# Kernel tuning notes

Measured on AMD Instinct MI355X. Metric: run time of the kernel, lower is better.

## Reference

```python
import jax, jax.numpy as jnp
import numpy as np

D_MODEL = 1024
N_HEADS = 16
HEAD_DIM = D_MODEL // N_HEADS
SEQ_LEN = 2048
D_FF = 4 * D_MODEL
LCC_SCALE = 0.1
LN_EPS = 1e-5
NORM_EPS = 1e-12  # F.normalize eps


def _layer_norm(x, g, b):
    mu = jnp.mean(x, axis=-1, keepdims=True)
    var = jnp.mean(jnp.square(x - mu), axis=-1, keepdims=True)
    return (x - mu) * jax.lax.rsqrt(var + LN_EPS) * g + b


def setup_inputs() -> dict:
    key = jax.random.key(0)
    ks = jax.random.split(key, 8)
    s = 0.02  # weight init scale
    return {
        "x": jax.random.normal(ks[0], (SEQ_LEN, D_MODEL), jnp.float32),
        "lcc_values": jax.random.uniform(ks[1], (SEQ_LEN,), jnp.float32),
        "w_qkv": jax.random.normal(ks[2], (D_MODEL, 3 * D_MODEL), jnp.float32) * s,
        "b_qkv": jnp.zeros((3 * D_MODEL,), jnp.float32),
        "w_out": jax.random.normal(ks[3], (D_MODEL, D_MODEL), jnp.float32) * s,
        "b_out": jnp.zeros((D_MODEL,), jnp.float32),
        "ln1_g": jnp.ones((D_MODEL,), jnp.float32),
        "ln1_b": jnp.zeros((D_MODEL,), jnp.float32),
        "ln2_g": jnp.ones((D_MODEL,), jnp.float32),
        "ln2_b": jnp.zeros((D_MODEL,), jnp.float32),
        "w_ff1": jax.random.normal(ks[4], (D_MODEL, D_FF), jnp.float32) * s,
        "b_ff1": jnp.zeros((D_FF,), jnp.float32),
        "w_ff2": jax.random.normal(ks[5], (D_FF, D_MODEL), jnp.float32) * s,
        "b_ff2": jnp.zeros((D_MODEL,), jnp.float32),
    }


def reference(x, lcc_values, w_qkv, b_qkv, w_out, b_out, ln1_g, ln1_b,
              ln2_g, ln2_b, w_ff1, b_ff1, w_ff2, b_ff2):
    L = x.shape[0]
    scaling = HEAD_DIM ** -0.5

    normed = _layer_norm(x, ln1_g, ln1_b)
    qkv = normed @ w_qkv + b_qkv                      # [L, 3D]
    qkv = qkv.reshape(L, 3, N_HEADS, HEAD_DIM)
    q = jnp.transpose(qkv[:, 0], (1, 0, 2))           # [H, L, d]
    k = jnp.transpose(qkv[:, 1], (1, 0, 2))
    v = jnp.transpose(qkv[:, 2], (1, 0, 2))

    # cosine attention: L2-normalize q, k
    q = q / jnp.maximum(jnp.linalg.norm(q, axis=-1, keepdims=True), NORM_EPS)
    k = k / jnp.maximum(jnp.linalg.norm(k, axis=-1, keepdims=True), NORM_EPS)
    q = q * scaling

    scores = jnp.einsum('hld,hmd->hlm', q, k)         # [H, L, L]
    bias = (lcc_values[:, None] + lcc_values[None, :]) * 0.5 * LCC_SCALE
    scores = jnp.clip(scores + bias[None], -10.0, 10.0)
    probs = jax.nn.softmax(scores, axis=-1)

    attn = jnp.einsum('hlm,hmd->hld', probs, v)       # [H, L, d]
    attn = jnp.transpose(attn, (1, 0, 2)).reshape(L, D_MODEL)
    x = x + (attn @ w_out + b_out)

    normed2 = _layer_norm(x, ln2_g, ln2_b)
    h = jax.nn.gelu(normed2 @ w_ff1 + b_ff1, approximate=False)
    x = x + (h @ w_ff2 + b_ff2)
    return x
```

## Files before the change

kernel.cpp:

```cpp
#include <hip/hip_runtime.h>
#include <hip/hip_bf16.h>

#define D_MODEL 1024
#define SEQ 2048
#define NH 16
#define HD 64
#define DFF 4096

typedef __attribute__((ext_vector_type(8))) __bf16 bf16x8;
typedef __attribute__((ext_vector_type(4))) float f32x4;

__device__ __forceinline__ unsigned short f2bf(float f) {
    union { float f; unsigned u; } v; v.f = f;
    unsigned r = v.u + 0x7fffu + ((v.u >> 16) & 1u);
    return (unsigned short)(r >> 16);
}
__device__ __forceinline__ unsigned pack2(float a, float b) {
    return (unsigned)f2bf(a) | ((unsigned)f2bf(b) << 16);
}
__device__ __forceinline__ float bf2f(unsigned short u) {
    union { unsigned u; float f; } v; v.u = ((unsigned)u) << 16;
    return v.f;
}
__device__ __forceinline__ bf16x8 ld_frag(const unsigned short* p) {
    union { uint4 u; bf16x8 b; } c;
    c.u = *(const uint4*)p;
    return c.b;
}

typedef __attribute__((address_space(3))) unsigned lds_u32;
typedef const __attribute__((address_space(1))) unsigned glob_u32;
__device__ __forceinline__ void gl_lds16(const unsigned short* g, unsigned short* l) {
    __builtin_amdgcn_global_load_lds((glob_u32*)g, (lds_u32*)l, 16, 0, 0);
}

#define MFMA16(a,b,c) __builtin_amdgcn_mfma_f32_16x16x32_bf16(a,b,c,0,0,0)

__global__ __launch_bounds__(256) void wcast_all(const float* __restrict__ wq, const float* __restrict__ wo,
                                                 const float* __restrict__ wf1, const float* __restrict__ wf2,
                                                 unsigned short* __restrict__ oq, unsigned short* __restrict__ oo,
                                                 unsigned short* __restrict__ of1, unsigned short* __restrict__ of2) {
    __shared__ unsigned short lt[64][72];
    int id = blockIdx.x;
    const float* W; unsigned short* O; int K, N, nb, kb;
    if (id < 768)       { W = wq;  O = oq;  K = 1024; N = 3072; nb = id % 48; kb = id / 48; }
    else if (id < 1024) { id -= 768;  W = wo;  O = oo;  K = 1024; N = 1024; nb = id & 15; kb = id >> 4; }
    else if (id < 2048) { id -= 1024; W = wf1; O = of1; K = 1024; N = 4096; nb = id & 63; kb = id >> 6; }
    else                { id -= 2048; W = wf2; O = of2; K = 4096; N = 1024; nb = id & 15; kb = id >> 4; }
    int t = threadIdx.x;
    int r = t >> 2, c0 = (t & 3) << 4;
    const float* src = W + (size_t)(kb*64 + r) * N + nb*64 + c0;
    float4 f0 = ((const float4*)src)[0];
    float4 f1 = ((const float4*)src)[1];
    float4 f2 = ((const float4*)src)[2];
    float4 f3 = ((const float4*)src)[3];
    unsigned* dst = (unsigned*)&lt[r][c0];
    dst[0]=pack2(f0.x,f0.y); dst[1]=pack2(f0.z,f0.w);
    dst[2]=pack2(f1.x,f1.y); dst[3]=pack2(f1.z,f1.w);
    dst[4]=pack2(f2.x,f2.y); dst[5]=pack2(f2.z,f2.w);
    dst[6]=pack2(f3.x,f3.y); dst[7]=pack2(f3.z,f3.w);
    __syncthreads();
    int n_ = t >> 2, k0 = (t & 3) << 4;
    unsigned obuf[8];
#pragma unroll
    for (int i = 0; i < 8; i++)
        obuf[i] = (unsigned)lt[k0 + 2*i][n_] | ((unsigned)lt[k0 + 2*i + 1][n_] << 16);
    unsigned short* out = O + (size_t)(nb*64 + n_) * K + kb*64 + k0;
    ((uint4*)out)[0] = *(uint4*)&obuf[0];
    ((uint4*)out)[1] = *(uint4*)&obuf[4];
}

__global__ __launch_bounds__(256) void ln_kernel(const float* __restrict__ x,
                                                 const float* __restrict__ g,
                                                 const float* __restrict__ b,
                                                 unsigned short* __restrict__ out) {
    int row = blockIdx.x, t = threadIdx.x;
    float4 v = ((const float4*)(x + (size_t)row * D_MODEL))[t];
    float s  = v.x + v.y + v.z + v.w;
    float sq = v.x*v.x + v.y*v.y + v.z*v.z + v.w*v.w;
#pragma unroll
    for (int m = 1; m < 64; m <<= 1) { s += __shfl_xor(s, m, 64); sq += __shfl_xor(sq, m, 64); }
    __shared__ float ls[4], lq[4];
    int wave = t >> 6, lane = t & 63;
    if (lane == 0) { ls[wave] = s; lq[wave] = sq; }
    __syncthreads();
    s  = ls[0]+ls[1]+ls[2]+ls[3];
    sq = lq[0]+lq[1]+lq[2]+lq[3];
    float mu  = s * (1.0f / D_MODEL);
    float var = sq * (1.0f / D_MODEL) - mu * mu;
    float rs  = rsqrtf(var + 1e-5f);
    int c = t * 4;
    float y0 = (v.x - mu) * rs * g[c+0] + b[c+0];
    float y1 = (v.y - mu) * rs * g[c+1] + b[c+1];
    float y2 = (v.z - mu) * rs * g[c+2] + b[c+2];
    float y3 = (v.w - mu) * rs * g[c+3] + b[c+3];
    unsigned* o = (unsigned*)(out + (size_t)row * D_MODEL + c);
    o[0] = pack2(y0, y1); o[1] = pack2(y2, y3);
}

__global__ __launch_bounds__(256) void reduce_ln(const float* __restrict__ x,
                                                 const float* __restrict__ bout,
                                                 const unsigned short* __restrict__ parts,
                                                 const float* __restrict__ g,
                                                 const float* __restrict__ b,
                                                 float* __restrict__ x1,
                                                 unsigned short* __restrict__ x2n) {
    int row = blockIdx.x, t = threadIdx.x;
    int i = row * 256 + t;
    float4 v = ((const float4*)x)[i];
    float4 bb = ((const float4*)bout)[t];
    v.x += bb.x; v.y += bb.y; v.z += bb.z; v.w += bb.w;
    ushort4 u0 = ((const ushort4*)parts)[i];
    ushort4 u1 = ((const ushort4*)(parts + (size_t)SEQ*D_MODEL))[i];
    v.x += bf2f(u0.x) + bf2f(u1.x);
    v.y += bf2f(u0.y) + bf2f(u1.y);
    v.z += bf2f(u0.z) + bf2f(u1.z);
    v.w += bf2f(u0.w) + bf2f(u1.w);
    ((float4*)x1)[i] = v;
    float s  = v.x + v.y + v.z + v.w;
    float sq = v.x*v.x + v.y*v.y + v.z*v.z + v.w*v.w;
#pragma unroll
    for (int m = 1; m < 64; m <<= 1) { s += __shfl_xor(s, m, 64); sq += __shfl_xor(sq, m, 64); }
    __shared__ float ls[4], lq[4];
    int wave = t >> 6, lane = t & 63;
    if (lane == 0) { ls[wave] = s; lq[wave] = sq; }
    __syncthreads();
    s  = ls[0]+ls[1]+ls[2]+ls[3];
    sq = lq[0]+lq[1]+lq[2]+lq[3];
    float mu  = s * (1.0f / D_MODEL);
    float var = sq * (1.0f / D_MODEL) - mu * mu;
    float rs  = rsqrtf(var + 1e-5f);
    int c = t * 4;
    float y0 = (v.x - mu) * rs * g[c+0] + b[c+0];
    float y1 = (v.y - mu) * rs * g[c+1] + b[c+1];
    float y2 = (v.z - mu) * rs * g[c+2] + b[c+2];
    float y3 = (v.w - mu) * rs * g[c+3] + b[c+3];
    unsigned* o = (unsigned*)(x2n + (size_t)row * D_MODEL + c);
    o[0] = pack2(y0, y1); o[1] = pack2(y2, y3);
}

__global__ __launch_bounds__(256) void reduce_ff2(const float* __restrict__ res,
                                                  const float* __restrict__ bias,
                                                  const unsigned short* __restrict__ parts,
                                                  float* __restrict__ out) {
    int i = blockIdx.x * 256 + threadIdx.x;
    float4 r = ((const float4*)res)[i];
    float4 b = ((const float4*)bias)[i & (D_MODEL/4 - 1)];
    r.x += b.x; r.y += b.y; r.z += b.z; r.w += b.w;
#pragma unroll
    for (int p = 0; p < 4; p++) {
        ushort4 u = ((const ushort4*)(parts + (size_t)p * SEQ * D_MODEL))[i];
        r.x += bf2f(u.x); r.y += bf2f(u.y); r.z += bf2f(u.z); r.w += bf2f(u.w);
    }
    ((float4*)out)[i] = r;
}

#define TMg 128
#define TNg 128
#define SMEM_U16 (2 * (TMg + TNg) * 64)
__device__ __forceinline__ void gemm_core(const unsigned short* __restrict__ A,
                                          const unsigned short* __restrict__ Bt,
                                          int K, int K0, int KS, int bm, int bn,
                                          unsigned short* smem, f32x4 acc[4][4],
                                          int wave, int lane) {
    constexpr int AI = 4, BI = 4, MI = 4, NI = 4;
    constexpr int HALF = (TMg + TNg) * 64;
    int quad = lane >> 4, lr = lane & 15;

    const unsigned short* pa[AI];
    int aoff[AI];
#pragma unroll
    for (int i = 0; i < AI; i++) {
        int rl = wave*32 + i*8 + (lane >> 3);
        int ss = (lane & 7) ^ (rl & 7);
        pa[i] = A + (size_t)(bm*TMg + rl) * K + K0 + ss*8;
        aoff[i] = (wave*32 + i*8) * 64;
    }
    const unsigned short* pb[BI];
    int boff[BI];
#pragma unroll
    for (int i = 0; i < BI; i++) {
        int rl = wave*32 + i*8 + (lane >> 3);
        int ss = (lane & 7) ^ (rl & 7);
        pb[i] = Bt + (size_t)(bn*TNg + rl) * K + K0 + ss*8;
        boff[i] = TMg*64 + (wave*32 + i*8) * 64;
    }

    int wr = (wave >> 1) * 64, wc = (wave & 1) * 64;
    int foA[2][MI], foB[2][NI];
#pragma unroll
    for (int i = 0; i < MI; i++) {
        int row = wr + i*16 + lr;
        foA[0][i] = row*64 + ((quad     ^ (row & 7)))*8;
        foA[1][i] = row*64 + (((quad+4) ^ (row & 7)))*8;
    }
#pragma unroll
    for (int j = 0; j < NI; j++) {
        int row = wc + j*16 + lr;
        foB[0][j] = TMg*64 + row*64 + ((quad     ^ (row & 7)))*8;
        foB[1][j] = TMg*64 + row*64 + (((quad+4) ^ (row & 7)))*8;
    }

#pragma unroll
    for (int i = 0; i < AI; i++) gl_lds16(pa[i], smem + aoff[i]);
#pragma unroll
    for (int i = 0; i < BI; i++) gl_lds16(pb[i], smem + boff[i]);

    int bo = 0;
    for (int kk = 0; kk < KS; kk += 64) {
        __syncthreads();
        if (kk + 64 < KS) {
            int nb = bo ^ HALF;
#pragma unroll
            for (int i = 0; i < AI; i++) gl_lds16(pa[i] + kk + 64, smem + nb + aoff[i]);
#pragma unroll
            for (int i = 0; i < BI; i++) gl_lds16(pb[i] + kk + 64, smem + nb + boff[i]);
        }
#pragma unroll
        for (int h = 0; h < 2; h++) {
            bf16x8 af[MI], bfr[NI];
#pragma unroll
            for (int i = 0; i < MI; i++) af[i]  = ld_frag(smem + bo + foA[h][i]);
#pragma unroll
            for (int j = 0; j < NI; j++) bfr[j] = ld_frag(smem + bo + foB[h][j]);
#pragma unroll
            for (int i = 0; i < MI; i++)
#pragma unroll
                for (int j = 0; j < NI; j++)
                    acc[i][j] = MFMA16(af[i], bfr[j], acc[i][j]);
        }
        bo ^= HALF;
    }
}

__device__ __forceinline__ void acc_init(f32x4 acc[4][4]) {
    f32x4 z = {0.f, 0.f, 0.f, 0.f};
#pragma unroll
    for (int i = 0; i < 4; i++)
#pragma unroll
        for (int j = 0; j < 4; j++) acc[i][j] = z;
}

__global__ __launch_bounds__(256) void k_gemm_qkv(const unsigned short* __restrict__ A,
                                                  const unsigned short* __restrict__ Bt,
                                                  const float* __restrict__ bias,
                                                  unsigned short* __restrict__ qn,
                                                  unsigned short* __restrict__ kn,
                                                  unsigned short* __restrict__ vt) {
    __shared__ unsigned short smem[SMEM_U16];
    int t = threadIdx.x;
    int bn = blockIdx.x, bm = blockIdx.y;
    int wave = t >> 6, lane = t & 63;
    int quad = lane >> 4, lr = lane & 15;
    f32x4 acc[4][4];
    acc_init(acc);
    gemm_core(A, Bt, 1024, 0, 1024, bm, bn, smem, acc, wave, lane);

    int wr = (wave >> 1) * 64, wc = (wave & 1) * 64;
    int sec = bn >> 3, hp = bn & 7;
    float bv[4];
#pragma unroll
    for (int j = 0; j < 4; j++) bv[j] = bias[bn*TNg + wc + j*16 + lr];
#pragma unroll
    for (int i = 0; i < 4; i++)
#pragma unroll
        for (int j = 0; j < 4; j++)
#pragma unroll
            for (int r = 0; r < 4; r++) acc[i][j][r] += bv[j];

    if (sec < 2) {
        int h = hp*2 + (wave & 1);
        unsigned short* dst = (sec == 0) ? qn : kn;
        float mul = (sec == 0) ? 0.125f : 1.0f;
#pragma unroll
        for (int i = 0; i < 4; i++)
#pragma unroll
            for (int r = 0; r < 4; r++) {
                float ss = 0.f;
#pragma unroll
                for (int j = 0; j < 4; j++) ss += acc[i][j][r]*acc[i][j][r];
                ss += __shfl_xor(ss, 1, 64); ss += __shfl_xor(ss, 2, 64);
                ss += __shfl_xor(ss, 4, 64); ss += __shfl_xor(ss, 8, 64);
                float scale = mul / fmaxf(sqrtf(ss), 1e-12f);
                int row = bm*TMg + wr + i*16 + quad*4 + r;
                size_t base = ((size_t)h*SEQ + row) * HD;
#pragma unroll
                for (int j = 0; j < 4; j++)
                    dst[base + j*16 + lr] = f2bf(acc[i][j][r] * scale);
            }
    } else {
        __syncthreads();
        unsigned short (*lv)[136] = (unsigned short (*)[136])smem;
#pragma unroll
        for (int i = 0; i < 4; i++)
#pragma unroll
            for (int j = 0; j < 4; j++)
#pragma unroll
                for (int r = 0; r < 4; r++)
                    lv[wc + j*16 + lr][wr + i*16 + quad*4 + r] = f2bf(acc[i][j][r]);
        __syncthreads();
        int d = t >> 1, l0 = (t & 1) * 64;
        unsigned short* ov = vt + ((size_t)(hp*128 + d)) * SEQ + bm*TMg + l0;
#pragma unroll
        for (int c = 0; c < 8; c++)
            ((uint4*)ov)[c] = *(uint4*)&lv[d][l0 + c*8];
    }
}

template<int SPLITK>
__device__ __forceinline__ void gemm_part(const unsigned short* A, const unsigned short* Bt,
                                          unsigned short* C, int M, int N, int K) {
    __shared__ unsigned short smem[SMEM_U16];
    int t = threadIdx.x;
    int bn = blockIdx.x, bm = blockIdx.y, kz = blockIdx.z;
    int wave = t >> 6, lane = t & 63;
    int quad = lane >> 4, lr = lane & 15;
    int KS = K / SPLITK;
    f32x4 acc[4][4];
    acc_init(acc);
    gemm_core(A, Bt, K, kz*KS, KS, bm, bn, smem, acc, wave, lane);
    int wr = (wave >> 1) * 64, wc = (wave & 1) * 64;
    unsigned short* P = C + (size_t)kz * M * N;
#pragma unroll
    for (int i = 0; i < 4; i++)
#pragma unroll
        for (int j = 0; j < 4; j++) {
            int row0 = bm*TMg + wr + i*16 + quad*4;
            int col  = bn*TNg + wc + j*16 + lr;
#pragma unroll
            for (int r = 0; r < 4; r++)
                P[(size_t)(row0 + r) * N + col] = f2bf(acc[i][j][r]);
        }
}
__global__ __launch_bounds__(256) void k_gemm_op(const unsigned short* A, const unsigned short* Bt,
                                                 unsigned short* C, int M, int N, int K) {
    gemm_part<2>(A, Bt, C, M, N, K);
}
__global__ __launch_bounds__(256) void k_gemm_ff2(const unsigned short* A, const unsigned short* Bt,
                                                  unsigned short* C, int M, int N, int K) {
    gemm_part<4>(A, Bt, C, M, N, K);
}

__global__ __launch_bounds__(256) void k_gemm_ff1(const unsigned short* __restrict__ A,
                                                  const unsigned short* __restrict__ Bt,
                                                  const float* __restrict__ bias,
                                                  unsigned short* __restrict__ C,
                                                  int M, int N, int K) {
    __shared__ unsigned short smem[SMEM_U16];
    int t = threadIdx.x;
    int bn = blockIdx.x, bm = blockIdx.y;
    int wave = t >> 6, lane = t & 63;
    int quad = lane >> 4, lr = lane & 15;
    f32x4 acc[4][4];
    acc_init(acc);
    gemm_core(A, Bt, K, 0, K, bm, bn, smem, acc, wave, lane);
    int wr = (wave >> 1) * 64, wc = (wave & 1) * 64;
#pragma unroll
    for (int i = 0; i < 4; i++)
#pragma unroll
        for (int j = 0; j < 4; j++) {
            int row0 = bm*TMg + wr + i*16 + quad*4;
            int col  = bn*TNg + wc + j*16 + lr;
            float bvv = bias[col];
#pragma unroll
            for (int r = 0; r < 4; r++) {
                float v = acc[i][j][r] + bvv;
                v = 0.5f * v * (1.0f + erff(v * 0.70710678118654752f));
                C[(size_t)(row0 + r) * N + col] = f2bf(v);
            }
        }
}

#define KSPLIT 2
#define KTILES (SEQ / 64 / KSPLIT)
__global__ __launch_bounds__(256) void attn_kernel(const unsigned short* __restrict__ qn,
                                                   const unsigned short* __restrict__ kn,
                                                   const unsigned short* __restrict__ vt,
                                                   const float* __restrict__ lcc,
                                                   float* __restrict__ num_ws,
                                                   float* __restrict__ den_ws) {
    __shared__ unsigned short lQP[64*64];
    __shared__ unsigned short lK[2][64*64];
    __shared__ unsigned short lV[2][64*64];
    int h = blockIdx.x, qb = blockIdx.y, kz = blockIdx.z;
    int t = threadIdx.x;
    int wave = t >> 6, lane = t & 63, quad = lane >> 4, lr = lane & 15;
    int r0 = lane >> 3;
    int ch = lane & 7;

    const unsigned short* kn0 = kn + (size_t)h*SEQ*HD + (size_t)kz*(SEQ/KSPLIT)*HD;
    const unsigned short* vt0 = vt + (size_t)h*HD*SEQ + kz*(SEQ/KSPLIT);
    const float* lcc0 = lcc + kz*(SEQ/KSPLIT);

#pragma unroll
    for (int i = 0; i < 2; i++) {
        int rl = wave*16 + i*8 + r0;
        int ss = ch ^ (rl & 7);
        gl_lds16(qn + ((size_t)h*SEQ + qb*64 + rl)*HD + ss*8, lQP + (wave*16 + i*8)*64);
        gl_lds16(kn0 + (size_t)rl*HD + ss*8,                  lK[0] + (wave*16 + i*8)*64);
        gl_lds16(vt0 + (size_t)rl*SEQ + ss*8,                 lV[0] + (wave*16 + i*8)*64);
    }
    __syncthreads();

    bf16x8 aq0 = ld_frag(lQP + (wave*16 + lr)*64 + ((quad     ^ (lr & 7)))*8);
    bf16x8 aq1 = ld_frag(lQP + (wave*16 + lr)*64 + (((quad+4) ^ (lr & 7)))*8);

    f32x4 z = {0.f, 0.f, 0.f, 0.f};
    f32x4 oacc[4]; oacc[0]=z; oacc[1]=z; oacc[2]=z; oacc[3]=z;
    float den[4] = {0.f, 0.f, 0.f, 0.f};

    int cur = 0;
    for (int kb = 0; kb < KTILES; kb++) {
        if (kb + 1 < KTILES) {
            int nxt = cur ^ 1;
#pragma unroll
            for (int i = 0; i < 2; i++) {
                int rl = wave*16 + i*8 + r0;
                int ss = ch ^ (rl & 7);
                gl_lds16(kn0 + (size_t)(kb+1)*64*HD + (size_t)rl*HD + ss*8,
                         lK[nxt] + (wave*16 + i*8)*64);
                gl_lds16(vt0 + (size_t)rl*SEQ + (kb+1)*64 + ss*8,
                         lV[nxt] + (wave*16 + i*8)*64);
            }
        }
        float lmv[4];
#pragma unroll
        for (int j = 0; j < 4; j++) lmv[j] = 0.05f * lcc0[kb*64 + j*16 + lr];

        __builtin_amdgcn_s_setprio(1);
        const unsigned short* Kc = lK[cur];
#pragma unroll
        for (int j = 0; j < 4; j++) {
            bf16x8 b0 = ld_frag(Kc + (j*16 + lr)*64 + ((quad     ^ (lr & 7)))*8);
            bf16x8 b1 = ld_frag(Kc + (j*16 + lr)*64 + (((quad+4) ^ (lr & 7)))*8);
            f32x4 s = z;
            s = MFMA16(aq0, b0, s);
            s = MFMA16(aq1, b1, s);
#pragma unroll
            for (int r = 0; r < 4; r++) {
                float p = __expf(s[r] + lmv[j]);
                den[r] += p;
                int prow = wave*16 + quad*4 + r;
                lQP[prow*64 + (((2*j + (lr >> 3)) ^ (prow & 7)))*8 + (lr & 7)] = f2bf(p);
            }
        }
        bf16x8 ap0 = ld_frag(lQP + (wave*16 + lr)*64 + ((quad     ^ (lr & 7)))*8);
        bf16x8 ap1 = ld_frag(lQP + (wave*16 + lr)*64 + (((quad+4) ^ (lr & 7)))*8);
        const unsigned short* Vc = lV[cur];
#pragma unroll
        for (int j2 = 0; j2 < 4; j2++) {
            bf16x8 b0 = ld_frag(Vc + (j2*16 + lr)*64 + ((quad     ^ (lr & 7)))*8);
            bf16x8 b1 = ld_frag(Vc + (j2*16 + lr)*64 + (((quad+4) ^ (lr & 7)))*8);
            oacc[j2] = MFMA16(ap0, b0, oacc[j2]);
            oacc[j2] = MFMA16(ap1, b1, oacc[j2]);
        }
        __builtin_amdgcn_s_setprio(0);
        __syncthreads();
        cur ^= 1;
    }
#pragma unroll
    for (int r = 0; r < 4; r++)
#pragma unroll
        for (int m = 1; m < 16; m <<= 1) den[r] += __shfl_xor(den[r], m, 64);

    float* nump = num_ws + (((size_t)(h*32 + qb)) * KSPLIT + kz) * 4096;
#pragma unroll
    for (int j2 = 0; j2 < 4; j2++)
#pragma unroll
        for (int r = 0; r < 4; r++)
            nump[(wave*16 + quad*4 + r) * 64 + j2*16 + lr] = oacc[j2][r];
    if (lr == 0) {
        float* denp = den_ws + (((size_t)(h*32 + qb)) * KSPLIT + kz) * 64;
#pragma unroll
        for (int r = 0; r < 4; r++) denp[wave*16 + quad*4 + r] = den[r];
    }
}

__global__ __launch_bounds__(256) void attn_comb(const float* __restrict__ num_ws,
                                                 const float* __restrict__ den_ws,
                                                 unsigned short* __restrict__ attn) {
    int hq = blockIdx.x;
    int h = hq >> 5, qb = hq & 31;
    int t = threadIdx.x;
    int row = t >> 2, col0 = (t & 3) << 4;
    const float* n0 = num_ws + ((size_t)hq * KSPLIT) * 4096 + row*64 + col0;
    const float* n1 = n0 + 4096;
    float d = den_ws[(size_t)hq * KSPLIT * 64 + row] + den_ws[((size_t)hq * KSPLIT + 1) * 64 + row];
    float inv = 1.0f / d;
    unsigned ob[8];
#pragma unroll
    for (int i = 0; i < 4; i++) {
        float4 a = ((const float4*)n0)[i];
        float4 b = ((const float4*)n1)[i];
        ob[2*i]   = pack2((a.x + b.x) * inv, (a.y + b.y) * inv);
        ob[2*i+1] = pack2((a.z + b.z) * inv, (a.w + b.w) * inv);
    }
    unsigned short* op = attn + (size_t)(qb*64 + row) * D_MODEL + h*64 + col0;
    ((uint4*)op)[0] = *(uint4*)&ob[0];
    ((uint4*)op)[1] = *(uint4*)&ob[4];
}

extern "C" void kernel_launch(void* const* d_in, const int* in_sizes, int n_in,
                              void* d_out, int out_size, void* d_ws, size_t ws_size,
                              hipStream_t stream) {
    const float* x      = (const float*)d_in[0];
    const float* lcc    = (const float*)d_in[1];
    const float* w_qkv  = (const float*)d_in[2];
    const float* b_qkv  = (const float*)d_in[3];
    const float* w_out  = (const float*)d_in[4];
    const float* b_out  = (const float*)d_in[5];
    const float* ln1_g  = (const float*)d_in[6];
    const float* ln1_b  = (const float*)d_in[7];
    const float* ln2_g  = (const float*)d_in[8];
    const float* ln2_b  = (const float*)d_in[9];
    const float* w_ff1  = (const float*)d_in[10];
    const float* b_ff1  = (const float*)d_in[11];
    const float* w_ff2  = (const float*)d_in[12];
    const float* b_ff2  = (const float*)d_in[13];

    char* ws = (char*)d_ws;
    unsigned short* wtq  = (unsigned short*)(ws);
    unsigned short* wto  = (unsigned short*)(ws + 6291456);
    unsigned short* wtf1 = (unsigned short*)(ws + 8388608);
    unsigned short* wtf2 = (unsigned short*)(ws + 16777216);
    unsigned short* xn   = (unsigned short*)(ws + 25165824);
    float*          x1   = (float*)(ws + 29360128);
    float*          numw = (float*)(ws + 29360128);
    float*          denw = (float*)(ws + 46137344);
    unsigned short* hbuf = (unsigned short*)(ws + 37748736);
    unsigned short* pOP  = (unsigned short*)(ws + 37748736);
    unsigned short* qnb  = (unsigned short*)(ws + 54525952);
    unsigned short* knb  = (unsigned short*)(ws + 58720256);
    unsigned short* vtb  = (unsigned short*)(ws + 62914560);
    unsigned short* pFF2 = (unsigned short*)(ws);
    unsigned short* attnb = xn;
    unsigned short* x2n  = qnb;
    float* outp = (float*)d_out;


    wcast_all<<<3072, 256, 0, stream>>>(w_qkv, w_out, w_ff1, w_ff2, wtq, wto, wtf1, wtf2);
    ln_kernel<<<SEQ, 256, 0, stream>>>(x, ln1_g, ln1_b, xn);
    k_gemm_qkv<<<dim3(24, 16), 256, 0, stream>>>(xn, wtq, b_qkv, qnb, knb, vtb);
    attn_kernel<<<dim3(16, 32, KSPLIT), 256, 0, stream>>>(qnb, knb, vtb, lcc, numw, denw);
    attn_comb<<<512, 256, 0, stream>>>(numw, denw, attnb);
    k_gemm_op<<<dim3(8, 16, 2), 256, 0, stream>>>(attnb, wto, pOP, SEQ, 1024, 1024);
    reduce_ln<<<SEQ, 256, 0, stream>>>(x, b_out, pOP, ln2_g, ln2_b, x1, x2n);
    k_gemm_ff1<<<dim3(32, 16), 256, 0, stream>>>(x2n, wtf1, b_ff1, hbuf, SEQ, 4096, 1024);
    k_gemm_ff2<<<dim3(8, 16, 4), 256, 0, stream>>>(hbuf, wtf2, pFF2, SEQ, 1024, 4096);
    reduce_ff2<<<SEQ*D_MODEL/1024, 256, 0, stream>>>(x1, b_ff2, pFF2, outp);
}
```

Measured before the change: 260.5 us.

## Use 4-stage K-32 shared-memory pipeline with explicit vmcnt waits in GEMM core

Result: slower. 269.4 us (+3.4%).

```diff
diff --git a/kernel.cpp b/kernel.cpp
--- a/kernel.cpp
+++ b/kernel.cpp
@@ -157,79 +157,71 @@
 
 #define TMg 128
 #define TNg 128
-#define SMEM_U16 (2 * (TMg + TNg) * 64)
+#define BKq 32
+#define BUF_U16 ((TMg + TNg) * BKq)
+#define SMEM_U16 (4 * BUF_U16)
 __device__ __forceinline__ void gemm_core(const unsigned short* __restrict__ A,
                                           const unsigned short* __restrict__ Bt,
                                           int K, int K0, int KS, int bm, int bn,
                                           unsigned short* smem, f32x4 acc[4][4],
                                           int wave, int lane) {
-    constexpr int AI = 4, BI = 4, MI = 4, NI = 4;
-    constexpr int HALF = (TMg + TNg) * 64;
     int quad = lane >> 4, lr = lane & 15;
-
-    const unsigned short* pa[AI];
-    int aoff[AI];
-#pragma unroll
-    for (int i = 0; i < AI; i++) {
-        int rl = wave*32 + i*8 + (lane >> 3);
-        int ss = (lane & 7) ^ (rl & 7);
-        pa[i] = A + (size_t)(bm*TMg + rl) * K + K0 + ss*8;
-        aoff[i] = (wave*32 + i*8) * 64;
-    }
-    const unsigned short* pb[BI];
-    int boff[BI];
-#pragma unroll
-    for (int i = 0; i < BI; i++) {
-        int rl = wave*32 + i*8 + (lane >> 3);
-        int ss = (lane & 7) ^ (rl & 7);
-        pb[i] = Bt + (size_t)(bn*TNg + rl) * K + K0 + ss*8;
-        boff[i] = TMg*64 + (wave*32 + i*8) * 64;
-    }
-
+    const unsigned short* pa[2]; const unsigned short* pb[2];
+    int aoff[2], boff[2];
+#pragma unroll
+    for (int i = 0; i < 2; i++) {
+        int rl = i*64 + wave*16 + (lane >> 2);
+        int sc = (lane & 3) ^ (rl & 3);
+        pa[i] = A + (size_t)(bm*TMg + rl) * K + K0 + sc*8;
+        pb[i] = Bt + (size_t)(bn*TNg + rl) * K + K0 + sc*8;
+        aoff[i] = (i*64 + wave*16) * BKq;
+        boff[i] = TMg*BKq + (i*64 + wave*16) * BKq;
+    }
     int wr = (wave >> 1) * 64, wc = (wave & 1) * 64;
-    int foA[2][MI], foB[2][NI];
-#pragma unroll
-    for (int i = 0; i < MI; i++) {
-        int row = wr + i*16 + lr;
-        foA[0][i] = row*64 + ((quad     ^ (row & 7)))*8;
-        foA[1][i] = row*64 + (((quad+4) ^ (row & 7)))*8;
-    }
-#pragma unroll
-    for (int j = 0; j < NI; j++) {
-        int row = wc + j*16 + lr;
-        foB[0][j] = TMg*64 + row*64 + ((quad     ^ (row & 7)))*8;
-        foB[1][j] = TMg*64 + row*64 + (((quad+4) ^ (row & 7)))*8;
-    }
-
-#pragma unroll
-    for (int i = 0; i < AI; i++) gl_lds16(pa[i], smem + aoff[i]);
-#pragma unroll
-    for (int i = 0; i < BI; i++) gl_lds16(pb[i], smem + boff[i]);
-
-    int bo = 0;
-    for (int kk = 0; kk < KS; kk += 64) {
-        __syncthreads();
-        if (kk + 64 < KS) {
-            int nb = bo ^ HALF;
-#pragma unroll
-            for (int i = 0; i < AI; i++) gl_lds16(pa[i] + kk + 64, smem + nb + aoff[i]);
-#pragma unroll
-            for (int i = 0; i < BI; i++) gl_lds16(pb[i] + kk + 64, smem + nb + boff[i]);
-        }
-#pragma unroll
-        for (int h = 0; h < 2; h++) {
-            bf16x8 af[MI], bfr[NI];
-#pragma unroll
-            for (int i = 0; i < MI; i++) af[i]  = ld_frag(smem + bo + foA[h][i]);
-#pragma unroll
-            for (int j = 0; j < NI; j++) bfr[j] = ld_frag(smem + bo + foB[h][j]);
-#pragma unroll
-            for (int i = 0; i < MI; i++)
-#pragma unroll
-                for (int j = 0; j < NI; j++)
-                    acc[i][j] = MFMA16(af[i], bfr[j], acc[i][j]);
-        }
-        bo ^= HALF;
+    int foA[4], foB[4];
+#pragma unroll
+    for (int i = 0; i < 4; i++) {
+        int ra = wr + i*16 + lr;
+        foA[i] = ra*BKq + (quad ^ (ra & 3))*8;
+        int rb = wc + i*16 + lr;
+        foB[i] = TMg*BKq + rb*BKq + (quad ^ (rb & 3))*8;
+    }
+    int T = KS >> 5;
+#pragma unroll
+    for (int t = 0; t < 3; t++) {
+        unsigned short* s = smem + t * BUF_U16;
+#pragma unroll
+        for (int i = 0; i < 2; i++) {
+            gl_lds16(pa[i] + t*BKq, s + aoff[i]);
+            gl_lds16(pb[i] + t*BKq, s + boff[i]);
+        }
+    }
+    for (int t = 0; t < T; t++) {
+        if (t < T - 2)      asm volatile("s_waitcnt vmcnt(8)" ::: "memory");
+        else if (t == T - 2) asm volatile("s_waitcnt vmcnt(4)" ::: "memory");
+        else                 asm volatile("s_waitcnt vmcnt(0)" ::: "memory");
+        __builtin_amdgcn_s_barrier();
+        if (t + 3 < T) {
+            unsigned short* s = smem + ((t + 3) & 3) * BUF_U16;
+#pragma unroll
+            for (int i = 0; i < 2; i++) {
+                gl_lds16(pa[i] + (t+3)*BKq, s + aoff[i]);
+                gl_lds16(pb[i] + (t+3)*BKq, s + boff[i]);
+            }
+        }
+        const unsigned short* s = smem + (t & 3) * BUF_U16;
+        bf16x8 af[4], bfr[4];
+#pragma unroll
+        for (int i = 0; i < 4; i++) af[i] = ld_frag(s + foA[i]);
+#pragma unroll
+        for (int j = 0; j < 4; j++) bfr[j] = ld_frag(s + foB[j]);
+        __builtin_amdgcn_s_setprio(1);
+#pragma unroll
+        for (int i = 0; i < 4; i++)
+#pragma unroll
+            for (int j = 0; j < 4; j++)
+                acc[i][j] = MFMA16(af[i], bfr[j], acc[i][j]);
+        __builtin_amdgcn_s_setprio(0);
     }
 }
 
```
